# Kernel optimization log

Measured on AMD Instinct MI355X. Metric: run time of the kernel, lower is better.

The kernel has to match this reference:

```python
import jax, jax.numpy as jnp
import numpy as np

N_QUBITS = 5
N_A = 1
N_LAYERS = 4
PATCH = 2 ** (N_QUBITS - N_A)  # 16

CNOT4 = jnp.array([[1, 0, 0, 0], [0, 1, 0, 0], [0, 0, 0, 1], [0, 0, 1, 0]], dtype=jnp.complex64)


def _ry(t):
    c = jnp.cos(t / 2).astype(jnp.complex64)
    s = jnp.sin(t / 2).astype(jnp.complex64)
    return jnp.stack([jnp.stack([c, -s]), jnp.stack([s, c])])


def _rot(phi, theta, omega):
    # PennyLane Rot = RZ(omega) RY(theta) RZ(phi)
    c = jnp.cos(theta / 2)
    s = jnp.sin(theta / 2)
    ep = jnp.exp(-0.5j * (phi + omega))  # e^{-i(phi+omega)/2}
    em = jnp.exp(-0.5j * (phi - omega))  # e^{-i(phi-omega)/2}
    return jnp.stack([jnp.stack([ep * c, -jnp.conj(em) * s]),
                      jnp.stack([em * s, jnp.conj(ep) * c])])


def _apply_1q(state, U, w):
    # contract U onto qubit axis w of state [2]*5
    s = jnp.tensordot(U, state, axes=(1, w))
    return jnp.moveaxis(s, 0, w)


def _apply_cnot(state, c, t):
    perm = jnp.moveaxis(state, (c, t), (0, 1))
    shp = perm.shape
    out = (CNOT4 @ perm.reshape(4, -1)).reshape(shp)
    return jnp.moveaxis(out, (0, 1), (c, t))


def _simulate(noise, w):
    # noise: [5], w: [4,5,3] -> normalized probs over first 16 basis states
    state = jnp.zeros((2,) * N_QUBITS, jnp.complex64).at[(0,) * N_QUBITS].set(1.0)
    for q in range(N_QUBITS):
        state = _apply_1q(state, _ry(noise[q]), q)
    for l in range(N_LAYERS):
        r = l % (N_QUBITS - 1) + 1  # StronglyEntanglingLayers default ranges
        for q in range(N_QUBITS):
            state = _apply_1q(state, _rot(w[l, q, 0], w[l, q, 1], w[l, q, 2]), q)
        for q in range(N_QUBITS):
            state = _apply_cnot(state, q, (q + r) % N_QUBITS)
    probs = jnp.abs(state.reshape(-1)) ** 2  # [32]
    p0 = probs[:PATCH] / jnp.sum(probs)  # partial measure: ancilla wire 4 == 0
    return p0 / jnp.max(p0)


def setup_inputs() -> dict:
    key = jax.random.key(0)
    k1, k2 = jax.random.split(key)
    B, G = 65536, 4
    x = jax.random.uniform(k1, (B, N_QUBITS), dtype=jnp.float32)
    weights = jax.random.uniform(k2, (G, N_LAYERS, N_QUBITS, 3), dtype=jnp.float32)  # q_delta=1
    return {"x": x, "weights": weights}


def reference(x, weights):
    sim_g = jax.vmap(_simulate, in_axes=(None, 0))   # over generators
    sim_bg = jax.vmap(sim_g, in_axes=(0, None))      # over batch
    out = sim_bg(x, weights)                         # [B, G, 16]
    return out.reshape(x.shape[0], -1).astype(jnp.float32)  # [B, G*16]
```

## Files before the change

kernel.cpp:

```cpp
#include <hip/hip_runtime.h>


#define NGEN 4
#define NLAY 4
#define NQ   5

typedef _Float16 half8 __attribute__((ext_vector_type(8)));
typedef float    f32x4 __attribute__((ext_vector_type(4)));

#define WAVE_SYNC()                                                  \
    do {                                                             \
        __builtin_amdgcn_wave_barrier();                             \
        asm volatile("s_waitcnt lgkmcnt(0)" ::: "memory");           \
        __builtin_amdgcn_wave_barrier();                             \
    } while (0)

__global__ __launch_bounds__(256) void pqg_fused(
    const float* __restrict__ x,
    const float* __restrict__ wts,
    float* __restrict__ out)
{
    __shared__ float gm[NGEN][NLAY * NQ * 8];
    __shared__ float Mr[NGEN][16 * 33];
    __shared__ float Mi[NGEN][16 * 33];
    __shared__ __align__(16) _Float16 afr[NGEN][512];
    __shared__ __align__(16) _Float16 afi[NGEN][512];
    __shared__ float scC[640];
    __shared__ float scS[640];

    const int t    = threadIdx.x;
    const int lane = t & 63;
    const int g    = t >> 6;
    const int b0   = blockIdx.x * 128;

    if (t < 160) {
        const float4 v = ((const float4*)(x + (size_t)b0 * 5))[t];
        scS[4 * t + 0] = __sinf(0.5f * v.x);  scC[4 * t + 0] = __cosf(0.5f * v.x);
        scS[4 * t + 1] = __sinf(0.5f * v.y);  scC[4 * t + 1] = __cosf(0.5f * v.y);
        scS[4 * t + 2] = __sinf(0.5f * v.z);  scC[4 * t + 2] = __cosf(0.5f * v.z);
        scS[4 * t + 3] = __sinf(0.5f * v.w);  scC[4 * t + 3] = __cosf(0.5f * v.w);
    }

    if (lane < NLAY * NQ) {
        const float* wp = wts + (g * (NLAY * NQ) + lane) * 3;
        const float phi = wp[0], theta = wp[1], omega = wp[2];
        const float a = 0.5f * (phi + omega);
        const float bb = 0.5f * (phi - omega);
        const float h = 0.5f * theta;
        const float sa = __sinf(a), ca = __cosf(a);
        const float sb = __sinf(bb), cb = __cosf(bb);
        const float st = __sinf(h), ct = __cosf(h);
        float* m = &gm[g][lane * 8];
        m[0] =  ca * ct;  m[1] = -sa * ct;
        m[2] = -cb * st;  m[3] = -sb * st;
        m[4] =  cb * st;  m[5] = -sb * st;
        m[6] =  ca * ct;  m[7] =  sa * ct;
    }

#pragma unroll
    for (int h = 0; h < 8; ++h) {
        const int idx = h * 64 + lane;
        const int r = idx >> 5, c = idx & 31;
        Mr[g][r * 33 + c] = (r == c) ? 1.0f : 0.0f;
        Mi[g][r * 33 + c] = 0.0f;
    }
    WAVE_SYNC();

    const int p  = lane & 15;
    const int rl = lane >> 4;

#pragma clang loop unroll(disable)
    for (int l = NLAY - 1; l >= 0; --l) {
        {
            int v0 = p, v1 = p + 16;
#pragma unroll
            for (int q = 0; q < NQ; ++q) {
                const int cb = 16 >> q;
                int tq = q + l + 1; if (tq >= NQ) tq -= NQ;
                const int tb = 16 >> tq;
                if (v0 & cb) v0 ^= tb;
                if (v1 & cb) v1 ^= tb;
            }
            float tr[8], ti[8];
#pragma unroll
            for (int r = 0; r < 4; ++r) {
                const int row = r * 4 + rl;
                tr[2 * r + 0] = Mr[g][row * 33 + v0];
                ti[2 * r + 0] = Mi[g][row * 33 + v0];
                tr[2 * r + 1] = Mr[g][row * 33 + v1];
                ti[2 * r + 1] = Mi[g][row * 33 + v1];
            }
            WAVE_SYNC();
#pragma unroll
            for (int r = 0; r < 4; ++r) {
                const int row = r * 4 + rl;
                Mr[g][row * 33 + p]      = tr[2 * r + 0];
                Mi[g][row * 33 + p]      = ti[2 * r + 0];
                Mr[g][row * 33 + p + 16] = tr[2 * r + 1];
                Mi[g][row * 33 + p + 16] = ti[2 * r + 1];
            }
            WAVE_SYNC();
        }
#pragma clang loop unroll(disable)
        for (int q = NQ - 1; q >= 0; --q) {
            const float* m = &gm[g][(l * NQ + q) * 8];
            const float u00r = m[0], u00i = m[1], u01r = m[2], u01i = m[3];
            const float u10r = m[4], u10i = m[5], u11r = m[6], u11i = m[7];
            const int sb = 16 >> q;
            const int lowm = sb - 1;
            const int i = ((p & ~lowm) << 1) | (p & lowm);
            const int j = i | sb;
#pragma unroll
            for (int r = 0; r < 4; ++r) {
                const int row = r * 4 + rl;
                const int ii = row * 33 + i, jj = row * 33 + j;
                const float ar = Mr[g][ii], ai = Mi[g][ii];
                const float br = Mr[g][jj], bi = Mi[g][jj];
                Mr[g][ii] = u00r * ar - u00i * ai + u10r * br - u10i * bi;
                Mi[g][ii] = u00r * ai + u00i * ar + u10r * bi + u10i * br;
                Mr[g][jj] = u01r * ar - u01i * ai + u11r * br - u11i * bi;
                Mi[g][jj] = u01r * ai + u01i * ar + u11r * bi + u11i * br;
            }
            WAVE_SYNC();
        }
    }

#pragma unroll
    for (int h = 0; h < 8; ++h) {
        const int idx = h * 64 + lane;
        const int k = idx >> 4, m = idx & 15;
        const int L = (k >> 3) * 16 + m;
        const int jj = k & 7;
        afr[g][L * 8 + jj] = (_Float16)Mr[g][m * 33 + k];
        afi[g][L * 8 + jj] = (_Float16)Mi[g][m * 33 + k];
    }

    __syncthreads();

    const int quad = lane >> 4;
    const int n    = lane & 15;

    const half8 Ar = *(const half8*)&afr[g][lane * 8];
    const half8 Ai = *(const half8*)&afi[g][lane * 8];

#pragma unroll
    for (int t8 = 0; t8 < 8; ++t8) {
        const int bl = t8 * 16 + n;
        const int b  = b0 + bl;
        const float* C = &scC[bl * 5];
        const float* S = &scS[bl * 5];

        const float f01 = ((quad & 2) ? S[0] : C[0]) * ((quad & 1) ? S[1] : C[1]);
        const float a0 = f01 * C[2], a1 = f01 * S[2];
        const float b00 = a0 * C[3], b01 = a0 * S[3];
        const float b10 = a1 * C[3], b11 = a1 * S[3];

        half8 Bf;
        Bf[0] = (_Float16)(b00 * C[4]);  Bf[1] = (_Float16)(b00 * S[4]);
        Bf[2] = (_Float16)(b01 * C[4]);  Bf[3] = (_Float16)(b01 * S[4]);
        Bf[4] = (_Float16)(b10 * C[4]);  Bf[5] = (_Float16)(b10 * S[4]);
        Bf[6] = (_Float16)(b11 * C[4]);  Bf[7] = (_Float16)(b11 * S[4]);

        f32x4 accR = {0.f, 0.f, 0.f, 0.f};
        f32x4 accI = {0.f, 0.f, 0.f, 0.f};
        accR = __builtin_amdgcn_mfma_f32_16x16x32_f16(Ar, Bf, accR, 0, 0, 0);
        accI = __builtin_amdgcn_mfma_f32_16x16x32_f16(Ai, Bf, accI, 0, 0, 0);

        const float p0 = accR[0] * accR[0] + accI[0] * accI[0];
        const float p1 = accR[1] * accR[1] + accI[1] * accI[1];
        const float p2 = accR[2] * accR[2] + accI[2] * accI[2];
        const float p3 = accR[3] * accR[3] + accI[3] * accI[3];

        float mx = fmaxf(fmaxf(p0, p1), fmaxf(p2, p3));
        mx = fmaxf(mx, __shfl_xor(mx, 16));
        mx = fmaxf(mx, __shfl_xor(mx, 32));
        const float inv = 1.0f / mx;

        const float4 o = make_float4(p0 * inv, p1 * inv, p2 * inv, p3 * inv);
        *(float4*)(out + (size_t)b * 64 + g * 16 + quad * 4) = o;
    }
}

extern "C" void kernel_launch(void* const* d_in, const int* in_sizes, int n_in,
                              void* d_out, int out_size, void* d_ws, size_t ws_size,
                              hipStream_t stream) {
    const float* x = (const float*)d_in[0];
    const float* w = (const float*)d_in[1];
    float* out = (float*)d_out;
    const int B = in_sizes[0] / NQ;

    pqg_fused<<<B / 128, 256, 0, stream>>>(x, w, out);
}
```

Measured before the change: 75.54 us.

## Keep circuit matrix in registers in MFMA fragment layout, drop block barrier

The 16x32 complex circuit matrix is now held per lane in registers, laid out as the MFMA A fragment. Gates on qubits 2-4 act within a lane's 8 registers, and LDS round-trips are kept only for the CNOT permutations and the qubit 0-1 gates. Each wave now computes its own sin/cos table for x, which removes the __syncthreads and the separate half-precision staging buffers. The cost is redundant transcendental work (four times per block), more LDS for the per-generator tables, and higher register pressure.

```diff
diff --git a/kernel.cpp b/kernel.cpp
--- a/kernel.cpp
+++ b/kernel.cpp
@@ -20,26 +20,17 @@
     const float* __restrict__ wts,
     float* __restrict__ out)
 {
-    __shared__ float gm[NGEN][NLAY * NQ * 8];
-    __shared__ float Mr[NGEN][16 * 33];
-    __shared__ float Mi[NGEN][16 * 33];
-    __shared__ __align__(16) _Float16 afr[NGEN][512];
-    __shared__ __align__(16) _Float16 afi[NGEN][512];
-    __shared__ float scC[640];
-    __shared__ float scS[640];
+    __shared__ float  gm[NGEN][NLAY * NQ * 8];
+    __shared__ float2 cs[NGEN][16 * 33];
+    __shared__ float  scS[NGEN][640];
+    __shared__ float  scC[NGEN][640];
 
     const int t    = threadIdx.x;
     const int lane = t & 63;
     const int g    = t >> 6;
     const int b0   = blockIdx.x * 128;
-
-    if (t < 160) {
-        const float4 v = ((const float4*)(x + (size_t)b0 * 5))[t];
-        scS[4 * t + 0] = __sinf(0.5f * v.x);  scC[4 * t + 0] = __cosf(0.5f * v.x);
-        scS[4 * t + 1] = __sinf(0.5f * v.y);  scC[4 * t + 1] = __cosf(0.5f * v.y);
-        scS[4 * t + 2] = __sinf(0.5f * v.z);  scC[4 * t + 2] = __cosf(0.5f * v.z);
-        scS[4 * t + 3] = __sinf(0.5f * v.w);  scC[4 * t + 3] = __cosf(0.5f * v.w);
-    }
+    const int cg   = lane >> 4;
+    const int m    = lane & 15;
 
     if (lane < NLAY * NQ) {
         const float* wp = wts + (g * (NLAY * NQ) + lane) * 3;
@@ -50,105 +41,118 @@
         const float sa = __sinf(a), ca = __cosf(a);
         const float sb = __sinf(bb), cb = __cosf(bb);
         const float st = __sinf(h), ct = __cosf(h);
-        float* m = &gm[g][lane * 8];
-        m[0] =  ca * ct;  m[1] = -sa * ct;
-        m[2] = -cb * st;  m[3] = -sb * st;
-        m[4] =  cb * st;  m[5] = -sb * st;
-        m[6] =  ca * ct;  m[7] =  sa * ct;
+        float* mm = &gm[g][lane * 8];
+        mm[0] =  ca * ct;  mm[1] = -sa * ct;
+        mm[2] = -cb * st;  mm[3] = -sb * st;
+        mm[4] =  cb * st;  mm[5] = -sb * st;
+        mm[6] =  ca * ct;  mm[7] =  sa * ct;
     }
 
 #pragma unroll
-    for (int h = 0; h < 8; ++h) {
-        const int idx = h * 64 + lane;
-        const int r = idx >> 5, c = idx & 31;
-        Mr[g][r * 33 + c] = (r == c) ? 1.0f : 0.0f;
-        Mi[g][r * 33 + c] = 0.0f;
+    for (int e = 0; e < 10; ++e) {
+        const int idx = e * 64 + lane;
+        const float tt = 0.5f * x[(size_t)b0 * 5 + idx];
+        scS[g][idx] = __sinf(tt);
+        scC[g][idx] = __cosf(tt);
     }
     WAVE_SYNC();
 
-    const int p  = lane & 15;
-    const int rl = lane >> 4;
+    float mr[8], mi[8];
+#pragma unroll
+    for (int j = 0; j < 8; ++j) {
+        mr[j] = (cg * 8 + j == m) ? 1.0f : 0.0f;
+        mi[j] = 0.0f;
+    }
 
-#pragma clang loop unroll(disable)
+#pragma unroll
     for (int l = NLAY - 1; l >= 0; --l) {
+#pragma unroll
+        for (int j = 0; j < 8; ++j)
+            cs[g][m * 33 + cg * 8 + j] = make_float2(mr[j], mi[j]);
+        WAVE_SYNC();
         {
-            int v0 = p, v1 = p + 16;
+            float2 tmp[8];
 #pragma unroll
-            for (int q = 0; q < NQ; ++q) {
-                const int cb = 16 >> q;
-                int tq = q + l + 1; if (tq >= NQ) tq -= NQ;
-                const int tb = 16 >> tq;
-                if (v0 & cb) v0 ^= tb;
-                if (v1 & cb) v1 ^= tb;
-            }
-            float tr[8], ti[8];
+            for (int j = 0; j < 8; ++j) {
+                int v = cg * 8 + j;
 #pragma unroll
-            for (int r = 0; r < 4; ++r) {
-                const int row = r * 4 + rl;
-                tr[2 * r + 0] = Mr[g][row * 33 + v0];
-                ti[2 * r + 0] = Mi[g][row * 33 + v0];
-                tr[2 * r + 1] = Mr[g][row * 33 + v1];
-                ti[2 * r + 1] = Mi[g][row * 33 + v1];
+                for (int q = 0; q < NQ; ++q) {
+                    const int cb = 16 >> q;
+                    int tq = q + l + 1; if (tq >= NQ) tq -= NQ;
+                    const int tb = 16 >> tq;
+                    if (v & cb) v ^= tb;
+                }
+                tmp[j] = cs[g][m * 33 + v];
             }
             WAVE_SYNC();
 #pragma unroll
-            for (int r = 0; r < 4; ++r) {
-                const int row = r * 4 + rl;
-                Mr[g][row * 33 + p]      = tr[2 * r + 0];
-                Mi[g][row * 33 + p]      = ti[2 * r + 0];
-                Mr[g][row * 33 + p + 16] = tr[2 * r + 1];
-                Mi[g][row * 33 + p + 16] = ti[2 * r + 1];
+            for (int j = 0; j < 8; ++j) { mr[j] = tmp[j].x; mi[j] = tmp[j].y; }
+        }
+
+#pragma unroll
+        for (int q = NQ - 1; q >= 2; --q) {
+            const float4 u0 = *(const float4*)&gm[g][(l * NQ + q) * 8];
+            const float4 u1 = *(const float4*)&gm[g][(l * NQ + q) * 8 + 4];
+            const float u00r = u0.x, u00i = u0.y, u01r = u0.z, u01i = u0.w;
+            const float u10r = u1.x, u10i = u1.y, u11r = u1.z, u11i = u1.w;
+            const int sb = 16 >> q;
+#pragma unroll
+            for (int ja = 0; ja < 8; ++ja) {
+                if (!(ja & sb)) {
+                    const int jb = ja | sb;
+                    const float ar = mr[ja], ai = mi[ja];
+                    const float br = mr[jb], bi = mi[jb];
+                    mr[ja] = u00r * ar - u00i * ai + u10r * br - u10i * bi;
+                    mi[ja] = u00r * ai + u00i * ar + u10r * bi + u10i * br;
+                    mr[jb] = u01r * ar - u01i * ai + u11r * br - u11i * bi;
+                    mi[jb] = u01r * ai + u01i * ar + u11r * bi + u11i * br;
+                }
             }
+        }
+
+#pragma unroll
+        for (int q = 1; q >= 0; --q) {
+            const float4 u0 = *(const float4*)&gm[g][(l * NQ + q) * 8];
+            const float4 u1 = *(const float4*)&gm[g][(l * NQ + q) * 8 + 4];
+            const float u00r = u0.x, u00i = u0.y, u01r = u0.z, u01i = u0.w;
+            const float u10r = u1.x, u10i = u1.y, u11r = u1.z, u11i = u1.w;
+            const int sb = 16 >> q;
+#pragma unroll
+            for (int j = 0; j < 8; ++j)
+                cs[g][m * 33 + cg * 8 + j] = make_float2(mr[j], mi[j]);
             WAVE_SYNC();
-        }
-#pragma clang loop unroll(disable)
-        for (int q = NQ - 1; q >= 0; --q) {
-            const float* m = &gm[g][(l * NQ + q) * 8];
-            const float u00r = m[0], u00i = m[1], u01r = m[2], u01i = m[3];
-            const float u10r = m[4], u10i = m[5], u11r = m[6], u11i = m[7];
-            const int sb = 16 >> q;
-            const int lowm = sb - 1;
-            const int i = ((p & ~lowm) << 1) | (p & lowm);
-            const int j = i | sb;
+            const int ibase = (cg * 8) & ~sb;
+            const int jbase = (cg * 8) |  sb;
+            const bool hi = ((cg * 8) & sb) != 0;
+            const float k0r = hi ? u01r : u00r, k0i = hi ? u01i : u00i;
+            const float k1r = hi ? u11r : u10r, k1i = hi ? u11i : u10i;
 #pragma unroll
-            for (int r = 0; r < 4; ++r) {
-                const int row = r * 4 + rl;
-                const int ii = row * 33 + i, jj = row * 33 + j;
-                const float ar = Mr[g][ii], ai = Mi[g][ii];
-                const float br = Mr[g][jj], bi = Mi[g][jj];
-                Mr[g][ii] = u00r * ar - u00i * ai + u10r * br - u10i * bi;
-                Mi[g][ii] = u00r * ai + u00i * ar + u10r * bi + u10i * br;
-                Mr[g][jj] = u01r * ar - u01i * ai + u11r * br - u11i * bi;
-                Mi[g][jj] = u01r * ai + u01i * ar + u11r * bi + u11i * br;
+            for (int j = 0; j < 8; ++j) {
+                const float2 A2 = cs[g][m * 33 + ibase + j];
+                const float2 B2 = cs[g][m * 33 + jbase + j];
+                mr[j] = k0r * A2.x - k0i * A2.y + k1r * B2.x - k1i * B2.y;
+                mi[j] = k0r * A2.y + k0i * A2.x + k1r * B2.y + k1i * B2.x;
             }
             WAVE_SYNC();
         }
     }
 
+    half8 Ar, Ai;
 #pragma unroll
-    for (int h = 0; h < 8; ++h) {
-        const int idx = h * 64 + lane;
-        const int k = idx >> 4, m = idx & 15;
-        const int L = (k >> 3) * 16 + m;
-        const int jj = k & 7;
-        afr[g][L * 8 + jj] = (_Float16)Mr[g][m * 33 + k];
-        afi[g][L * 8 + jj] = (_Float16)Mi[g][m * 33 + k];
+    for (int j = 0; j < 8; ++j) {
+        Ar[j] = (_Float16)mr[j];
+        Ai[j] = (_Float16)mi[j];
     }
 
-    __syncthreads();
-
-    const int quad = lane >> 4;
-    const int n    = lane & 15;
-
-    const half8 Ar = *(const half8*)&afr[g][lane * 8];
-    const half8 Ai = *(const half8*)&afi[g][lane * 8];
+    const int quad = cg;
+    const int n    = m;
 
 #pragma unroll
     for (int t8 = 0; t8 < 8; ++t8) {
         const int bl = t8 * 16 + n;
         const int b  = b0 + bl;
-        const float* C = &scC[bl * 5];
-        const float* S = &scS[bl * 5];
+        const float* C = &scC[g][bl * 5];
+        const float* S = &scS[g][bl * 5];
 
         const float f01 = ((quad & 2) ? S[0] : C[0]) * ((quad & 1) ? S[1] : C[1]);
         const float a0 = f01 * C[2], a1 = f01 * S[2];
```

After: 68.98 us. -8.7%, faster.
